# Performance work log

Measured on AMD Instinct MI355X. Metric: run time of the kernel, lower is better.

## Reference

```python
import jax, jax.numpy as jnp
import numpy as np

D_MODEL = 1024
NUM_HEADS = 16
HEAD_DIM = D_MODEL // NUM_HEADS


def setup_inputs() -> dict:
    key = jax.random.key(0)
    k_x, k_qkv, k_o = jax.random.split(key, 3)
    B, L = 2, 2048
    x = jax.random.normal(k_x, (B, L, D_MODEL), dtype=jnp.float32)
    # torch Linear weight [out, in]; y = x @ W.T. Scale ~ kaiming-uniform-ish.
    s = 1.0 / np.sqrt(D_MODEL)
    W_qkv = jax.random.uniform(k_qkv, (3 * D_MODEL, D_MODEL), dtype=jnp.float32, minval=-s, maxval=s)
    W_o = jax.random.uniform(k_o, (D_MODEL, D_MODEL), dtype=jnp.float32, minval=-s, maxval=s)
    return {"x": x, "W_qkv": W_qkv, "W_o": W_o}


def reference(x, W_qkv, W_o):
    B, L, D = x.shape
    H, dk = NUM_HEADS, HEAD_DIM
    qkv = (x @ W_qkv.T).reshape(B, L, 3, H, dk)
    q = qkv[:, :, 0].transpose(0, 2, 1, 3)  # [B,H,L,dk]
    k = qkv[:, :, 1].transpose(0, 2, 1, 3)
    v = qkv[:, :, 2].transpose(0, 2, 1, 3)
    scale = 1.0 / np.sqrt(dk).astype(np.float32)
    attn = jnp.einsum('bhqd,bhkd->bhqk', q, k) * scale  # [B,H,L,L]
    causal = jnp.tril(jnp.ones((L, L), dtype=bool))
    attn = jnp.where(causal, attn, -jnp.inf)
    attn = jax.nn.softmax(attn, axis=-1)
    y = jnp.einsum('bhqk,bhkd->bhqd', attn, v)  # [B,H,L,dk]
    y = y.transpose(0, 2, 1, 3).reshape(B, L, D)
    return y @ W_o.T
```

## Files before the change

### kernel.cpp

```cpp
#include <hip/hip_runtime.h>

typedef unsigned short u16;
typedef unsigned int   u32;

typedef __attribute__((ext_vector_type(4)))  float  f32x4;
typedef __attribute__((ext_vector_type(16))) float  f32x16;
typedef __attribute__((ext_vector_type(4)))  u32    u32x4;
typedef __attribute__((ext_vector_type(8)))  __bf16 bf16x8;

#define B_  2
#define L_  2048
#define H_  16

__device__ static inline u16 f2bf(float f) {
  u32 u = __builtin_bit_cast(u32, f);
  u32 r = u + 0x7fffu + ((u >> 16) & 1u);
  return (u16)(r >> 16);
}
__device__ static inline u32 pack2(float a, float b) {
  return (u32)f2bf(a) | ((u32)f2bf(b) << 16);
}
__device__ static inline u32 pack2t(float a, float b) {
  return __builtin_amdgcn_perm(__builtin_bit_cast(u32, b),
                               __builtin_bit_cast(u32, a), 0x07060302u);
}

__device__ static inline void swap32p(u32& a, u32& b) {
  auto r = __builtin_amdgcn_permlane32_swap(a, b, false, false);
  a = r[0]; b = r[1];
}

__device__ static inline void gload_lds16(const u16* g, u16* lds) {
  __builtin_amdgcn_global_load_lds((__attribute__((address_space(1))) void*)(g),
                                   (__attribute__((address_space(3))) void*)(lds),
                                   16, 0, 0);
}

__global__ __launch_bounds__(256) void cvt3_kernel(
    const float4* __restrict__ a, uint2* __restrict__ ao, int na,
    const float4* __restrict__ b, uint2* __restrict__ bo, int nb,
    const float4* __restrict__ c, uint2* __restrict__ co, int nc)
{
  const int step = gridDim.x * 256;
  constexpr int nq = 1024 * 1024 / 4;
  for (int i = blockIdx.x * 256 + threadIdx.x; i < na; i += step) {
    float4 f = a[i];
    ao[i] = make_uint2(pack2(f.x, f.y), pack2(f.z, f.w));
  }
  for (int i = blockIdx.x * 256 + threadIdx.x; i < nb; i += step) {
    float4 f = b[i];
    const float s = (i < nq) ? 0.125f : 1.0f;
    bo[i] = make_uint2(pack2(f.x * s, f.y * s), pack2(f.z * s, f.w * s));
  }
  for (int i = blockIdx.x * 256 + threadIdx.x; i < nc; i += step) {
    float4 f = c[i];
    co[i] = make_uint2(pack2(f.x, f.y), pack2(f.z, f.w));
  }
}

template <bool OUT_F32, int NT, bool DBUF>
__global__ __launch_bounds__(256) void gemm_bt_kernel(
    const u16* __restrict__ A, const u16* __restrict__ Bt, void* __restrict__ Cv,
    const int K, const int N)
{
  constexpr int NB = DBUF ? 2 : 1;
  constexpr int JT = NT / 32;
  __shared__ __attribute__((aligned(16))) u16 Al[NB][128 * 64];
  __shared__ __attribute__((aligned(16))) u16 Bl[NB][NT * 64];

  const int tid  = threadIdx.x;
  const int w    = tid >> 6;
  const int lane = tid & 63;
  const int m0 = blockIdx.y * 128;
  const int n0 = blockIdx.x * NT;
  const int mo = (w >> 1) * 64;
  const int no = (w & 1) * (NT / 2);

  const int sr8  = lane >> 3;
  const int scol = (((lane & 7) ^ ((lane >> 3) & 7)) * 8);

  const f32x4 zero = {0.f, 0.f, 0.f, 0.f};
  f32x4 acc[4][JT];
  #pragma unroll
  for (int i = 0; i < 4; ++i)
    #pragma unroll
    for (int j = 0; j < JT; ++j) acc[i][j] = zero;

  const int frow = lane & 15;
  const int fg   = lane >> 4;

  auto stage = [&](int buf, int k0) {
    #pragma unroll
    for (int inst = 0; inst < 4; ++inst) {
      const int r = w * 32 + inst * 8 + sr8;
      gload_lds16(A + (size_t)(m0 + r) * K + k0 + scol, &Al[buf][(w * 32 + inst * 8) * 64]);
    }
    #pragma unroll
    for (int inst = 0; inst < NT / 32; ++inst) {
      const int r = w * (NT / 4) + inst * 8 + sr8;
      gload_lds16(Bt + (size_t)(n0 + r) * K + k0 + scol, &Bl[buf][(w * (NT / 4) + inst * 8) * 64]);
    }
  };

  if (DBUF) stage(0, 0);

  int cur = 0;
  for (int k0 = 0; k0 < K; k0 += 64) {
    __syncthreads();
    if (DBUF) {
      if (k0 + 64 < K) stage(cur ^ 1, k0 + 64);
    } else {
      stage(0, k0);
      __syncthreads();
    }
    #pragma unroll
    for (int ks = 0; ks < 2; ++ks) {
      const int fco = ((ks * 4 + fg) ^ (frow & 7)) * 8;
      bf16x8 af[4], bfr[JT];
      #pragma unroll
      for (int i = 0; i < 4; ++i)
        af[i] = *(const bf16x8*)&Al[cur][(mo + i * 16 + frow) * 64 + fco];
      #pragma unroll
      for (int j = 0; j < JT; ++j)
        bfr[j] = *(const bf16x8*)&Bl[cur][(no + j * 16 + frow) * 64 + fco];
      #pragma unroll
      for (int i = 0; i < 4; ++i)
        #pragma unroll
        for (int j = 0; j < JT; ++j)
          acc[i][j] = __builtin_amdgcn_mfma_f32_16x16x32_bf16(af[i], bfr[j], acc[i][j], 0, 0, 0);
    }
    if (DBUF) cur ^= 1;
  }

  const int crow0 = m0 + mo + (lane >> 4) * 4;
  const int ccol0 = n0 + no + (lane & 15);
  #pragma unroll
  for (int i = 0; i < 4; ++i)
    #pragma unroll
    for (int j = 0; j < JT; ++j)
      #pragma unroll
      for (int r = 0; r < 4; ++r) {
        const size_t idx = (size_t)(crow0 + i * 16 + r) * N + (ccol0 + j * 16);
        if (OUT_F32) ((float*)Cv)[idx] = acc[i][j][r];
        else         ((u16*)Cv)[idx]   = f2bf(acc[i][j][r]);
      }
}

__global__ __launch_bounds__(512, 2) void gemm256_kernel(
    const u16* __restrict__ A, const u16* __restrict__ Bt, u16* __restrict__ C,
    const int K, const int N)
{
  __shared__ __attribute__((aligned(16))) u16 Al[2][256 * 64];
  __shared__ __attribute__((aligned(16))) u16 Bl[2][256 * 64];

  const int tid  = threadIdx.x;
  const int w    = tid >> 6;
  const int lane = tid & 63;
  const int wm   = w >> 2;
  const int wn   = w & 3;
  const int frow = lane & 15;
  const int fg   = lane >> 4;
  const int sr8  = lane >> 3;
  const int scol = (((lane & 7) ^ ((lane >> 3) & 7)) * 8);

  const int nbx = N >> 8;
  int id = blockIdx.y * gridDim.x + blockIdx.x;
  const int cpx = (gridDim.x * gridDim.y) >> 3;
  id = (id & 7) * cpx + (id >> 3);
  const int m0 = (id / nbx) * 256;
  const int n0 = (id % nbx) * 256;

  f32x4 acc[8][4];
  #pragma unroll
  for (int i = 0; i < 8; ++i)
    #pragma unroll
    for (int j = 0; j < 4; ++j) acc[i][j] = (f32x4){0.f, 0.f, 0.f, 0.f};

  auto stageA = [&](int buf, int h, int k0) {
    #pragma unroll
    for (int j = 0; j < 2; ++j) {
      const int rbase = h * 128 + w * 16 + j * 8;
      gload_lds16(A + (size_t)(m0 + rbase + sr8) * K + k0 + scol, &Al[buf][rbase * 64]);
    }
  };
  auto stageB = [&](int buf, int h, int k0) {
    #pragma unroll
    for (int j = 0; j < 2; ++j) {
      const int rbase = h * 128 + w * 16 + j * 8;
      gload_lds16(Bt + (size_t)(n0 + rbase + sr8) * K + k0 + scol, &Bl[buf][rbase * 64]);
    }
  };

#define PHASE(CBUF, Q, STAGE_STMT)                                              \
  {                                                                             \
    constexpr int mq = (Q) >> 1, nq = (Q) & 1;                                  \
    bf16x8 af[2][4];                                                            \
    bf16x8 bfr[2][2];                                                           \
    _Pragma("unroll")                                                           \
    for (int ks = 0; ks < 2; ++ks) {                                            \
      const int fco = ((ks * 4 + fg) ^ (frow & 7)) * 8;                         \
      _Pragma("unroll")                                                         \
      for (int i = 0; i < 4; ++i)                                               \
        af[ks][i] = *(const bf16x8*)&Al[CBUF][(wm * 128 + mq * 64 + i * 16 + frow) * 64 + fco]; \
      _Pragma("unroll")                                                         \
      for (int j = 0; j < 2; ++j)                                               \
        bfr[ks][j] = *(const bf16x8*)&Bl[CBUF][(wn * 64 + nq * 32 + j * 16 + frow) * 64 + fco]; \
    }                                                                           \
    STAGE_STMT;                                                                 \
    __builtin_amdgcn_s_barrier();                                               \
    asm volatile("s_waitcnt lgkmcnt(0)" ::: "memory");                          \
    __builtin_amdgcn_sched_barrier(0);                                          \
    __builtin_amdgcn_s_setprio(1);                                              \
    _Pragma("unroll")                                                           \
    for (int ks = 0; ks < 2; ++ks)                                              \
      _Pragma("unroll")                                                         \
      for (int i = 0; i < 4; ++i)                                               \
        _Pragma("unroll")                                                       \
        for (int j = 0; j < 2; ++j)                                             \
          acc[mq * 4 + i][nq * 2 + j] = __builtin_amdgcn_mfma_f32_16x16x32_bf16(\
              af[ks][i], bfr[ks][j], acc[mq * 4 + i][nq * 2 + j], 0, 0, 0);     \
    __builtin_amdgcn_s_setprio(0);                                              \
  }

  const int KT = K >> 6;

  stageA(0, 0, 0); stageA(0, 1, 0);
  stageB(0, 0, 0); stageB(0, 1, 0);
  if (KT > 1) {
    stageA(1, 0, 64);
    asm volatile("s_waitcnt vmcnt(2)" ::: "memory");
  } else {
    asm volatile("s_waitcnt vmcnt(0)" ::: "memory");
  }
  __builtin_amdgcn_s_barrier();

  for (int t = 0; t < KT; ++t) {
    const int  c  = t & 1;
    const bool h1 = (t + 1) < KT;
    const int  kn = (t + 1) << 6;

    PHASE(c, 0, if (h1) stageA(c ^ 1, 1, kn));
    __builtin_amdgcn_s_barrier();
    PHASE(c, 1, if (h1) stageB(c ^ 1, 0, kn));
    __builtin_amdgcn_s_barrier();
    PHASE(c, 2, if (h1) stageB(c ^ 1, 1, kn));
    __builtin_amdgcn_s_barrier();
    PHASE(c, 3, );
    if (t + 2 < KT) {
      stageA(c, 0, (t + 2) << 6);
      asm volatile("s_waitcnt vmcnt(2)" ::: "memory");
    } else {
      asm volatile("s_waitcnt vmcnt(0)" ::: "memory");
    }
    __builtin_amdgcn_s_barrier();
  }
#undef PHASE

  const int crow0 = m0 + wm * 128 + fg * 4;
  const int ccol0 = n0 + wn * 64 + frow;
  #pragma unroll
  for (int i = 0; i < 8; ++i)
    #pragma unroll
    for (int j = 0; j < 4; ++j)
      #pragma unroll
      for (int r = 0; r < 4; ++r)
        C[(size_t)(crow0 + i * 16 + r) * N + (ccol0 + j * 16)] = f2bf(acc[i][j][r]);
}

__global__ __launch_bounds__(256, 4) void attn_mfma_kernel(const u16* __restrict__ qkv,
                                                           u16* __restrict__ y)
{
  __shared__ __attribute__((aligned(16))) unsigned char smem[32768];

  const int tid  = threadIdx.x;
  const int w    = tid >> 6;
  const int lane = tid & 63;
  const int ql   = lane & 31;
  const int hi   = lane >> 5;
  const int qh   = w >> 1;
  const int kh   = w & 1;
  const int bh   = blockIdx.x;
  const int bb   = bh >> 4;
  const int hh   = bh & 15;
  const size_t rb = (size_t)bb * L_;

  const int a  = blockIdx.y & 7;
  const int cc = blockIdx.y >> 3;
  const int qt = (cc == 0) ? a : (cc == 1) ? (31 - a) : (cc == 2) ? (8 + a) : (23 - a);

  u16* Kt   = (u16*)(smem);
  u32* Vtd  = (u32*)(smem + 16384);
  float* Ocmb = (float*)smem;
  float* Lcmb = (float*)(smem + 16384);

  const int kkp = lane & 31;
  const int dc  = 2 * w + (lane >> 5);

  const int ksr = w * 16 + (lane >> 3);
  const int ksc = (((lane & 7) ^ ((lane >> 3) & 7)) * 8);

  const int q0 = qt * 64;
  const int qb = q0 + qh * 32;
  const int n  = qt + 1;

  bf16x8 qf[4];
  #pragma unroll
  for (int s = 0; s < 4; ++s)
    qf[s] = *(const bf16x8*)(qkv + (rb + qb + ql) * 3072 + hh * 64 + s * 16 + 8 * hi);

  f32x16 oacc0 = {}, oacc1 = {};
  float lsum = 0.f;

  auto stageK = [&](int buf, int kt) {
    #pragma unroll
    for (int inst = 0; inst < 2; ++inst)
      gload_lds16(qkv + (rb + kt + ksr + inst * 8) * 3072 + 1024 + hh * 64 + ksc,
                  &Kt[buf * 4096 + (w * 16 + inst * 8) * 64]);
  };
  auto loadV = [&](int kt, uint4& va, uint4& vb) {
    const u16* vp = qkv + (rb + kt + 2 * kkp) * 3072 + 2048 + hh * 64 + dc * 8;
    va = *(const uint4*)vp;
    vb = *(const uint4*)(vp + 3072);
  };
  auto writeV = [&](int buf, uint4 va, uint4 vb) {
    u16 a16[8], b16[8];
    *(uint4*)a16 = va; *(uint4*)b16 = vb;
    #pragma unroll
    for (int i = 0; i < 8; ++i)
      Vtd[buf * 2048 + (dc * 8 + i) * 32 + 4 * ((kkp >> 2) ^ i) + (kkp & 3)] =
          (u32)a16[i] | ((u32)b16[i] << 16);
  };

  {
    stageK(0, 0);
    uint4 va, vb;
    loadV(0, va, vb);
    writeV(0, va, vb);
  }

  int cur = 0;
  for (int it = 0; it < n; ++it) {
    __syncthreads();

    const int  kt       = it * 64;
    const bool havenext = (it + 1) < n;
    uint4 va, vb;
    if (havenext) {
      stageK(cur ^ 1, kt + 64);
      loadV(kt + 64, va, vb);
    }

    const bool diag = (kt == q0);
    if (!(diag && kh > qh)) {
      f32x16 sacc = {};
      __builtin_amdgcn_s_setprio(1);
      #pragma unroll
      for (int s = 0; s < 4; ++s) {
        bf16x8 kf = *(const bf16x8*)&Kt[cur * 4096 + (kh * 32 + ql) * 64 +
                                        (((2 * s + hi) ^ (ql & 7)) * 8)];
        sacc = __builtin_amdgcn_mfma_f32_32x32x16_bf16(kf, qf[s], sacc, 0, 0, 0);
      }
      __builtin_amdgcn_s_setprio(0);

      u32 u[8];
      if (diag && kh == qh) {
        #pragma unroll
        for (int j = 0; j < 8; ++j) {
          const int r0  = 2 * j;
          const int k0r = (r0 & 3) + 8 * (r0 >> 2) + 4 * hi;
          const float p0 = (k0r     > ql) ? 0.f : __expf(sacc[r0]);
          const float p1 = (k0r + 1 > ql) ? 0.f : __expf(sacc[r0 + 1]);
          lsum += p0 + p1;
          u[j] = pack2t(p0, p1);
        }
      } else {
        #pragma unroll
        for (int j = 0; j < 8; ++j) {
          const float p0 = __expf(sacc[2 * j]);
          const float p1 = __expf(sacc[2 * j + 1]);
          lsum += p0 + p1;
          u[j] = pack2t(p0, p1);
        }
      }

      swap32p(u[0], u[2]); swap32p(u[1], u[3]);
      swap32p(u[4], u[6]); swap32p(u[5], u[7]);
      const bf16x8 pf0 = __builtin_bit_cast(bf16x8, (u32x4){u[0], u[1], u[2], u[3]});
      const bf16x8 pf1 = __builtin_bit_cast(bf16x8, (u32x4){u[4], u[5], u[6], u[7]});

      __builtin_amdgcn_s_setprio(1);
      #pragma unroll
      for (int dt = 0; dt < 2; ++dt) {
        f32x16& oa = dt ? oacc1 : oacc0;
        const int d = dt * 32 + ql;
        bf16x8 vf0 = *(const bf16x8*)&Vtd[cur * 2048 + d * 32 + 4 * ((4 * kh + hi) ^ (ql & 7))];
        oa = __builtin_amdgcn_mfma_f32_32x32x16_bf16(vf0, pf0, oa, 0, 0, 0);
        bf16x8 vf1 = *(const bf16x8*)&Vtd[cur * 2048 + d * 32 + 4 * ((4 * kh + 2 + hi) ^ (ql & 7))];
        oa = __builtin_amdgcn_mfma_f32_32x32x16_bf16(vf1, pf1, oa, 0, 0, 0);
      }
      __builtin_amdgcn_s_setprio(0);
    }

    if (havenext) writeV(cur ^ 1, va, vb);
    cur ^= 1;
  }

  lsum += __shfl_xor(lsum, 32);

  __syncthreads();
  if (kh == 1) {
    #pragma unroll
    for (int dt = 0; dt < 2; ++dt)
      #pragma unroll
      for (int rq = 0; rq < 4; ++rq) {
        const f32x16& oa = dt ? oacc1 : oacc0;
        *(f32x4*)&Ocmb[(qh * 8 + dt * 4 + rq) * 256 + lane * 4] =
            (f32x4){oa[4 * rq], oa[4 * rq + 1], oa[4 * rq + 2], oa[4 * rq + 3]};
      }
    if (hi == 0) Lcmb[qh * 32 + ql] = lsum;
  }
  __syncthreads();
  if (kh == 0) {
    const float inv = 1.f / (lsum + Lcmb[qh * 32 + ql]);
    u16* yp = y + (rb + qb + ql) * 1024 + hh * 64;
    #pragma unroll
    for (int dt = 0; dt < 2; ++dt)
      #pragma unroll
      for (int rq = 0; rq < 4; ++rq) {
        const f32x16& oa = dt ? oacc1 : oacc0;
        const f32x4 oc = *(const f32x4*)&Ocmb[(qh * 8 + dt * 4 + rq) * 256 + lane * 4];
        const float v0 = (oa[4 * rq]     + oc[0]) * inv;
        const float v1 = (oa[4 * rq + 1] + oc[1]) * inv;
        const float v2 = (oa[4 * rq + 2] + oc[2]) * inv;
        const float v3 = (oa[4 * rq + 3] + oc[3]) * inv;
        *(uint2*)(yp + dt * 32 + 8 * rq + 4 * hi) = make_uint2(pack2(v0, v1), pack2(v2, v3));
      }
  }
}

extern "C" void kernel_launch(void* const* d_in, const int* in_sizes, int n_in,
                              void* d_out, int out_size, void* d_ws, size_t ws_size,
                              hipStream_t stream)
{
  const float* x    = (const float*)d_in[0];
  const float* Wqkv = (const float*)d_in[1];
  const float* Wo   = (const float*)d_in[2];
  float* out = (float*)d_out;

  u16* xb    = (u16*)d_ws;
  u16* Wqkvb = xb    + (size_t)4096 * 1024;
  u16* Wob   = Wqkvb + (size_t)3072 * 1024;
  u16* qkv   = Wob   + (size_t)1024 * 1024;
  u16* y     = qkv   + (size_t)4096 * 3072;

  cvt3_kernel<<<dim3(2048), dim3(256), 0, stream>>>(
      (const float4*)x,    (uint2*)xb,    4096 * 1024 / 4,
      (const float4*)Wqkv, (uint2*)Wqkvb, 3072 * 1024 / 4,
      (const float4*)Wo,   (uint2*)Wob,   1024 * 1024 / 4);

  gemm256_kernel<<<dim3(3072 / 256, 4096 / 256), dim3(512), 0, stream>>>(
      xb, Wqkvb, qkv, 1024, 3072);
  attn_mfma_kernel<<<dim3(B_ * H_, 32), dim3(256), 0, stream>>>(qkv, y);
  gemm_bt_kernel<true, 64, true><<<dim3(1024 / 64, 4096 / 128), dim3(256), 0, stream>>>(
      y, Wob, out, 1024, 1024);
}
```

Measured before the change: 167.3 us.

## Use 256x192 tiles in QKV GEMM with single-stage prefetch and hoisted B fragments

The QKV projection GEMM moves from 256x256 to 256x192 output tiles, giving 256 blocks instead of 192 so the CUs are better covered. The staged A/B half-tile loads interleaved across phases are replaced by one whole-tile prefetch per K step, and B fragments are loaded once per K step and reused across the four M phases. This trades the finer-grained load overlap and the deeper A prefetch for better load balance and fewer LDS reads, and adds a full vmcnt(0) wait at the end of each step.

```diff
diff --git a/kernel.cpp b/kernel.cpp
--- a/kernel.cpp
+++ b/kernel.cpp
@@ -151,7 +151,7 @@
     const int K, const int N)
 {
   __shared__ __attribute__((aligned(16))) u16 Al[2][256 * 64];
-  __shared__ __attribute__((aligned(16))) u16 Bl[2][256 * 64];
+  __shared__ __attribute__((aligned(16))) u16 Bl[2][192 * 64];
 
   const int tid  = threadIdx.x;
   const int w    = tid >> 6;
@@ -163,50 +163,43 @@
   const int sr8  = lane >> 3;
   const int scol = (((lane & 7) ^ ((lane >> 3) & 7)) * 8);
 
-  const int nbx = N >> 8;
+  const int nbx = N / 192;
   int id = blockIdx.y * gridDim.x + blockIdx.x;
   const int cpx = (gridDim.x * gridDim.y) >> 3;
   id = (id & 7) * cpx + (id >> 3);
   const int m0 = (id / nbx) * 256;
-  const int n0 = (id % nbx) * 256;
-
-  f32x4 acc[8][4];
+  const int n0 = (id % nbx) * 192;
+
+  f32x4 acc[8][3];
   #pragma unroll
   for (int i = 0; i < 8; ++i)
     #pragma unroll
-    for (int j = 0; j < 4; ++j) acc[i][j] = (f32x4){0.f, 0.f, 0.f, 0.f};
-
-  auto stageA = [&](int buf, int h, int k0) {
-    #pragma unroll
-    for (int j = 0; j < 2; ++j) {
-      const int rbase = h * 128 + w * 16 + j * 8;
+    for (int j = 0; j < 3; ++j) acc[i][j] = (f32x4){0.f, 0.f, 0.f, 0.f};
+
+  auto stageAll = [&](int buf, int k0) {
+    #pragma unroll
+    for (int j = 0; j < 4; ++j) {
+      const int rbase = w * 32 + j * 8;
       gload_lds16(A + (size_t)(m0 + rbase + sr8) * K + k0 + scol, &Al[buf][rbase * 64]);
     }
+    #pragma unroll
+    for (int j = 0; j < 3; ++j) {
+      const int rbase = w * 24 + j * 8;
+      gload_lds16(Bt + (size_t)(n0 + rbase + sr8) * K + k0 + scol, &Bl[buf][rbase * 64]);
+    }
   };
-  auto stageB = [&](int buf, int h, int k0) {
-    #pragma unroll
-    for (int j = 0; j < 2; ++j) {
-      const int rbase = h * 128 + w * 16 + j * 8;
-      gload_lds16(Bt + (size_t)(n0 + rbase + sr8) * K + k0 + scol, &Bl[buf][rbase * 64]);
-    }
-  };
-
-#define PHASE(CBUF, Q, STAGE_STMT)                                              \
+
+#define DO_PHASE(Q, EXTRA)                                                      \
   {                                                                             \
-    constexpr int mq = (Q) >> 1, nq = (Q) & 1;                                  \
-    bf16x8 af[2][4];                                                            \
-    bf16x8 bfr[2][2];                                                           \
+    bf16x8 af[2][2];                                                            \
     _Pragma("unroll")                                                           \
     for (int ks = 0; ks < 2; ++ks) {                                            \
       const int fco = ((ks * 4 + fg) ^ (frow & 7)) * 8;                         \
       _Pragma("unroll")                                                         \
-      for (int i = 0; i < 4; ++i)                                               \
-        af[ks][i] = *(const bf16x8*)&Al[CBUF][(wm * 128 + mq * 64 + i * 16 + frow) * 64 + fco]; \
-      _Pragma("unroll")                                                         \
-      for (int j = 0; j < 2; ++j)                                               \
-        bfr[ks][j] = *(const bf16x8*)&Bl[CBUF][(wn * 64 + nq * 32 + j * 16 + frow) * 64 + fco]; \
+      for (int i = 0; i < 2; ++i)                                               \
+        af[ks][i] = *(const bf16x8*)&Al[c][(wm * 128 + ((Q) * 2 + i) * 16 + frow) * 64 + fco]; \
     }                                                                           \
-    STAGE_STMT;                                                                 \
+    EXTRA;                                                                      \
     __builtin_amdgcn_s_barrier();                                               \
     asm volatile("s_waitcnt lgkmcnt(0)" ::: "memory");                          \
     __builtin_amdgcn_sched_barrier(0);                                          \
@@ -214,54 +207,53 @@
     _Pragma("unroll")                                                           \
     for (int ks = 0; ks < 2; ++ks)                                              \
       _Pragma("unroll")                                                         \
-      for (int i = 0; i < 4; ++i)                                               \
+      for (int i = 0; i < 2; ++i)                                               \
         _Pragma("unroll")                                                       \
-        for (int j = 0; j < 2; ++j)                                             \
-          acc[mq * 4 + i][nq * 2 + j] = __builtin_amdgcn_mfma_f32_16x16x32_bf16(\
-              af[ks][i], bfr[ks][j], acc[mq * 4 + i][nq * 2 + j], 0, 0, 0);     \
+        for (int j = 0; j < 3; ++j)                                             \
+          acc[(Q) * 2 + i][j] = __builtin_amdgcn_mfma_f32_16x16x32_bf16(        \
+              af[ks][i], bfr[ks][j], acc[(Q) * 2 + i][j], 0, 0, 0);             \
     __builtin_amdgcn_s_setprio(0);                                              \
   }
 
   const int KT = K >> 6;
 
-  stageA(0, 0, 0); stageA(0, 1, 0);
-  stageB(0, 0, 0); stageB(0, 1, 0);
-  if (KT > 1) {
-    stageA(1, 0, 64);
-    asm volatile("s_waitcnt vmcnt(2)" ::: "memory");
-  } else {
-    asm volatile("s_waitcnt vmcnt(0)" ::: "memory");
-  }
+  stageAll(0, 0);
+  asm volatile("s_waitcnt vmcnt(0)" ::: "memory");
   __builtin_amdgcn_s_barrier();
 
   for (int t = 0; t < KT; ++t) {
     const int  c  = t & 1;
     const bool h1 = (t + 1) < KT;
     const int  kn = (t + 1) << 6;
-
-    PHASE(c, 0, if (h1) stageA(c ^ 1, 1, kn));
+    bf16x8 bfr[2][3];
+
+    DO_PHASE(0, {
+      _Pragma("unroll")
+      for (int ks = 0; ks < 2; ++ks) {
+        const int fco = ((ks * 4 + fg) ^ (frow & 7)) * 8;
+        _Pragma("unroll")
+        for (int j = 0; j < 3; ++j)
+          bfr[ks][j] = *(const bf16x8*)&Bl[c][(wn * 48 + j * 16 + frow) * 64 + fco];
+      }
+      if (h1) stageAll(c ^ 1, kn);
+    });
     __builtin_amdgcn_s_barrier();
-    PHASE(c, 1, if (h1) stageB(c ^ 1, 0, kn));
+    DO_PHASE(1, );
     __builtin_amdgcn_s_barrier();
-    PHASE(c, 2, if (h1) stageB(c ^ 1, 1, kn));
+    DO_PHASE(2, );
     __builtin_amdgcn_s_barrier();
-    PHASE(c, 3, );
-    if (t + 2 < KT) {
-      stageA(c, 0, (t + 2) << 6);
-      asm volatile("s_waitcnt vmcnt(2)" ::: "memory");
-    } else {
-      asm volatile("s_waitcnt vmcnt(0)" ::: "memory");
-    }
+    DO_PHASE(3, );
+    asm volatile("s_waitcnt vmcnt(0)" ::: "memory");
     __builtin_amdgcn_s_barrier();
   }
-#undef PHASE
+#undef DO_PHASE
 
   const int crow0 = m0 + wm * 128 + fg * 4;
-  const int ccol0 = n0 + wn * 64 + frow;
+  const int ccol0 = n0 + wn * 48 + frow;
   #pragma unroll
   for (int i = 0; i < 8; ++i)
     #pragma unroll
-    for (int j = 0; j < 4; ++j)
+    for (int j = 0; j < 3; ++j)
       #pragma unroll
       for (int r = 0; r < 4; ++r)
         C[(size_t)(crow0 + i * 16 + r) * N + (ccol0 + j * 16)] = f2bf(acc[i][j][r]);
@@ -458,7 +450,7 @@
       (const float4*)Wqkv, (uint2*)Wqkvb, 3072 * 1024 / 4,
       (const float4*)Wo,   (uint2*)Wob,   1024 * 1024 / 4);
 
-  gemm256_kernel<<<dim3(3072 / 256, 4096 / 256), dim3(512), 0, stream>>>(
+  gemm256_kernel<<<dim3(3072 / 192, 4096 / 256), dim3(512), 0, stream>>>(
       xb, Wqkvb, qkv, 1024, 3072);
   attn_mfma_kernel<<<dim3(B_ * H_, 32), dim3(256), 0, stream>>>(qkv, y);
   gemm_bt_kernel<true, 64, true><<<dim3(1024 / 64, 4096 / 128), dim3(256), 0, stream>>>(
```

Result: faster. 162.7 us (-2.8%).
